# Optimization experiments

Hardware: AMD Instinct MI355X
Metric: run time of the kernel (lower is better)

Reference implementation:

```python
import jax, jax.numpy as jnp
import numpy as np

NOISE_MULTIPLIER = 1.1
L2_NORM_CLIP = 1.0


def setup_inputs() -> dict:
    key = jax.random.key(0)
    inputs = jax.random.normal(key, (16384, 1024), dtype=jnp.float32)
    return {"inputs": inputs}


def reference(inputs) -> jnp.ndarray:
    B = inputs.shape[0]
    embed_flat = inputs.reshape(B, -1)  # [B, D]
    # per-sample L2 norm; scale = 1 / max(norm / clip, 1)
    norm = jnp.linalg.norm(embed_flat, ord=2, axis=-1)  # [B]
    scale = 1.0 / jnp.maximum(norm / L2_NORM_CLIP, 1.0)  # [B]
    # row-wise scaling == diag(scale) @ embed_flat, without the O(B^2) matmul
    clipped = (embed_flat * scale[:, None]).reshape(inputs.shape)
    noise_key = jax.random.key(42)
    noise = NOISE_MULTIPLIER * L2_NORM_CLIP * jax.random.normal(
        noise_key, inputs.shape, dtype=inputs.dtype
    )
    return clipped + noise
```

## Files before the change

kernel.cpp:

```cpp
#include <hip/hip_runtime.h>
#include <cstdint>
#include <cstddef>

#define ROWS 16384
#define COLS 1024

__device__ __forceinline__ uint32_t rotl32(uint32_t x, int r) {
    return __builtin_amdgcn_alignbit(x, x, 32 - r);
}

struct TF4 { uint32_t a0,a1,b0,b1,c0,c1,d0,d1; };

__device__ __forceinline__ void tf_round4(TF4& s, int r) {
    s.a0 += s.a1; s.b0 += s.b1; s.c0 += s.c1; s.d0 += s.d1;
    s.a1 = rotl32(s.a1, r) ^ s.a0;
    s.b1 = rotl32(s.b1, r) ^ s.b0;
    s.c1 = rotl32(s.c1, r) ^ s.c0;
    s.d1 = rotl32(s.d1, r) ^ s.d0;
}

__device__ __forceinline__ void inj4(TF4& s, uint32_t k0, uint32_t k1) {
    s.a0 += k0; s.b0 += k0; s.c0 += k0; s.d0 += k0;
    s.a1 += k1; s.b1 += k1; s.c1 += k1; s.d1 += k1;
}

__device__ __forceinline__ void inj4_x1(TF4& s, uint32_t k1) {
    s.a1 += k1; s.b1 += k1; s.c1 += k1; s.d1 += k1;
}

__device__ __forceinline__ uint4 threefry_bits4(uint32_t i) {
    const uint32_t ks1 = 42u;
    const uint32_t ks2 = 0x1BD11BF0u;

    TF4 s;
    s.a1 = i + 42u;  s.a0 = s.a1;
    s.b1 = i + 43u;  s.b0 = s.b1;
    s.c1 = i + 44u;  s.c0 = s.c1;
    s.d1 = i + 45u;  s.d0 = s.d1;
    s.a1 = rotl32(s.a1, 13) ^ s.a0;
    s.b1 = rotl32(s.b1, 13) ^ s.b0;
    s.c1 = rotl32(s.c1, 13) ^ s.c0;
    s.d1 = rotl32(s.d1, 13) ^ s.d0;
    tf_round4(s, 15); tf_round4(s, 26); tf_round4(s, 6);
    inj4(s, ks1, ks2 + 1u);
    tf_round4(s, 17); tf_round4(s, 29); tf_round4(s, 16); tf_round4(s, 24);
    inj4(s, ks2, 2u);
    tf_round4(s, 13); tf_round4(s, 15); tf_round4(s, 26); tf_round4(s, 6);
    inj4_x1(s, ks1 + 3u);
    tf_round4(s, 17); tf_round4(s, 29); tf_round4(s, 16); tf_round4(s, 24);
    inj4(s, ks1, ks2 + 4u);
    tf_round4(s, 13); tf_round4(s, 15); tf_round4(s, 26); tf_round4(s, 6);
    inj4(s, ks2, 5u);

    return make_uint4(s.a0 ^ s.a1, s.b0 ^ s.b1, s.c0 ^ s.c1, s.d0 ^ s.d1);
}

__device__ __noinline__ float noise_tail(float y) {
    float w = fmaf(-0.69314718f, y, 2.5f);
    float s = __builtin_amdgcn_sqrtf(w) - 3.0f;
    float q = -3.1146030e-04f;
    q = fmaf(q, s, 1.5704224e-04f);
    q = fmaf(q, s, 2.0990855e-03f);
    q = fmaf(q, s, -5.7144932e-03f);
    q = fmaf(q, s, 8.9285939e-03f);
    q = fmaf(q, s, -1.1857797e-02f);
    q = fmaf(q, s, 1.4683435e-02f);
    q = fmaf(q, s, 1.5582439e+00f);
    q = fmaf(q, s, 4.4070777e+00f);
    return q;
}

__device__ __forceinline__ float4 noise4(uint32_t idx0) {
    uint4 b = threefry_bits4(idx0);

    float f0 = (float)(b.x >> 9);
    float f1 = (float)(b.y >> 9);
    float f2 = (float)(b.z >> 9);
    float f3 = (float)(b.w >> 9);

    const float S = 2.3841858e-07f;
    const float M = -0.99999994f;
    float v0 = fmaf(f0, S, M), v1 = fmaf(f1, S, M),
          v2 = fmaf(f2, S, M), v3 = fmaf(f3, S, M);

    float t0 = fmaf(-v0, v0, 1.0f), t1 = fmaf(-v1, v1, 1.0f),
          t2 = fmaf(-v2, v2, 1.0f), t3 = fmaf(-v3, v3, 1.0f);

    const float C = 3.6067376f;
    float y0 = __log2f(t0) + C, y1 = __log2f(t1) + C,
          y2 = __log2f(t2) + C, y3 = __log2f(t3) + C;

    const float K4 = 7.84913e-05f, K3 = 6.49511e-04f, K2 = -3.12243e-03f,
                K1 = -2.6594862e-01f, K0 = 2.3356449e+00f;
    float p0 = fmaf(K4, y0, K3), p1 = fmaf(K4, y1, K3),
          p2 = fmaf(K4, y2, K3), p3 = fmaf(K4, y3, K3);
    p0 = fmaf(p0, y0, K2); p1 = fmaf(p1, y1, K2);
    p2 = fmaf(p2, y2, K2); p3 = fmaf(p3, y3, K2);
    p0 = fmaf(p0, y0, K1); p1 = fmaf(p1, y1, K1);
    p2 = fmaf(p2, y2, K1); p3 = fmaf(p3, y3, K1);
    p0 = fmaf(p0, y0, K0); p1 = fmaf(p1, y1, K0);
    p2 = fmaf(p2, y2, K0); p3 = fmaf(p3, y3, K0);

    if (y0 <= -3.6067376f) p0 = noise_tail(y0);
    if (y1 <= -3.6067376f) p1 = noise_tail(y1);
    if (y2 <= -3.6067376f) p2 = noise_tail(y2);
    if (y3 <= -3.6067376f) p3 = noise_tail(y3);

    float4 n;
    n.x = p0 * v0; n.y = p1 * v1; n.z = p2 * v2; n.w = p3 * v3;
    return n;
}

__device__ __forceinline__ float ssq4(float4 a) {
    return fmaf(a.x, a.x, fmaf(a.y, a.y, fmaf(a.z, a.z, a.w * a.w)));
}

__global__ void __launch_bounds__(256)
gaussian_dp_kernel(const float* __restrict__ in, float* __restrict__ out) {
    const int wid  = threadIdx.x >> 6;
    const int lane = threadIdx.x & 63;
    const int r    = (blockIdx.x << 2) + wid;

    const float4* inR = reinterpret_cast<const float4*>(in + (size_t)r * COLS);
    float4 a0 = inR[lane];
    float4 a1 = inR[lane + 64];
    float4 a2 = inR[lane + 128];
    float4 a3 = inR[lane + 192];

    const uint32_t base = ((uint32_t)r << 10) + ((uint32_t)lane << 2);

    float4 n0 = noise4(base);
    float4 n1 = noise4(base + 256u);
    float4 n2 = noise4(base + 512u);
    float4 n3 = noise4(base + 768u);

    float ssq = (ssq4(a0) + ssq4(a1)) + (ssq4(a2) + ssq4(a3));

    #pragma unroll
    for (int off = 32; off > 0; off >>= 1) {
        ssq += __shfl_xor(ssq, off, 64);
    }

    const float scale = 1.0f / fmaxf(__builtin_amdgcn_sqrtf(ssq), 1.0f);

    float4* outR = reinterpret_cast<float4*>(out + (size_t)r * COLS);

    float4 o;
    o.x = fmaf(a0.x, scale, n0.x); o.y = fmaf(a0.y, scale, n0.y);
    o.z = fmaf(a0.z, scale, n0.z); o.w = fmaf(a0.w, scale, n0.w);
    outR[lane] = o;

    o.x = fmaf(a1.x, scale, n1.x); o.y = fmaf(a1.y, scale, n1.y);
    o.z = fmaf(a1.z, scale, n1.z); o.w = fmaf(a1.w, scale, n1.w);
    outR[lane + 64] = o;

    o.x = fmaf(a2.x, scale, n2.x); o.y = fmaf(a2.y, scale, n2.y);
    o.z = fmaf(a2.z, scale, n2.z); o.w = fmaf(a2.w, scale, n2.w);
    outR[lane + 128] = o;

    o.x = fmaf(a3.x, scale, n3.x); o.y = fmaf(a3.y, scale, n3.y);
    o.z = fmaf(a3.z, scale, n3.z); o.w = fmaf(a3.w, scale, n3.w);
    outR[lane + 192] = o;
}

extern "C" void kernel_launch(void* const* d_in, const int* in_sizes, int n_in,
                              void* d_out, int out_size, void* d_ws, size_t ws_size,
                              hipStream_t stream) {
    const float* in = (const float*)d_in[0];
    float* out = (float*)d_out;
    gaussian_dp_kernel<<<ROWS / 4, 256, 0, stream>>>(in, out);
}
```

Before: 40.50 us.

## Two-pass row processing with rolled loops and folded log offset in noise polynomial

The kernel now reads each row once to compute the sum of squares, then re-reads the input (expected to hit cache) and generates noise one float4 group at a time in a non-unrolled loop. This shrinks live state and register pressure, aiming for higher occupancy. It also folds the +C offset of the log2 value into the polynomial coefficients and the tail threshold, removing one add per element. The costs are a second read of the input and less instruction-level parallelism, since noise generation no longer overlaps the loads.

```diff
diff --git a/kernel.cpp b/kernel.cpp
--- a/kernel.cpp
+++ b/kernel.cpp
@@ -55,8 +55,8 @@
     return make_uint4(s.a0 ^ s.a1, s.b0 ^ s.b1, s.c0 ^ s.c1, s.d0 ^ s.d1);
 }
 
-__device__ __noinline__ float noise_tail(float y) {
-    float w = fmaf(-0.69314718f, y, 2.5f);
+__device__ __noinline__ float noise_tail(float L) {
+    float w = -0.69314718f * L;
     float s = __builtin_amdgcn_sqrtf(w) - 3.0f;
     float q = -3.1146030e-04f;
     q = fmaf(q, s, 1.5704224e-04f);
@@ -86,25 +86,24 @@
     float t0 = fmaf(-v0, v0, 1.0f), t1 = fmaf(-v1, v1, 1.0f),
           t2 = fmaf(-v2, v2, 1.0f), t3 = fmaf(-v3, v3, 1.0f);
 
-    const float C = 3.6067376f;
-    float y0 = __log2f(t0) + C, y1 = __log2f(t1) + C,
-          y2 = __log2f(t2) + C, y3 = __log2f(t3) + C;
+    float L0 = __log2f(t0), L1 = __log2f(t1),
+          L2 = __log2f(t2), L3 = __log2f(t3);
 
-    const float K4 = 7.84913e-05f, K3 = 6.49511e-04f, K2 = -3.12243e-03f,
-                K1 = -2.6594862e-01f, K0 = 2.3356449e+00f;
-    float p0 = fmaf(K4, y0, K3), p1 = fmaf(K4, y1, K3),
-          p2 = fmaf(K4, y2, K3), p3 = fmaf(K4, y3, K3);
-    p0 = fmaf(p0, y0, K2); p1 = fmaf(p1, y1, K2);
-    p2 = fmaf(p2, y2, K2); p3 = fmaf(p3, y3, K2);
-    p0 = fmaf(p0, y0, K1); p1 = fmaf(p1, y1, K1);
-    p2 = fmaf(p2, y2, K1); p3 = fmaf(p3, y3, K1);
-    p0 = fmaf(p0, y0, K0); p1 = fmaf(p1, y1, K0);
-    p2 = fmaf(p2, y2, K0); p3 = fmaf(p3, y3, K0);
+    const float K4 = 7.84913e-05f, K3 = 1.781908e-03f, K2 = 1.0031874e-02f,
+                K1 = -2.4839395e-01f, K0 = 1.3795727e+00f;
+    float p0 = fmaf(K4, L0, K3), p1 = fmaf(K4, L1, K3),
+          p2 = fmaf(K4, L2, K3), p3 = fmaf(K4, L3, K3);
+    p0 = fmaf(p0, L0, K2); p1 = fmaf(p1, L1, K2);
+    p2 = fmaf(p2, L2, K2); p3 = fmaf(p3, L3, K2);
+    p0 = fmaf(p0, L0, K1); p1 = fmaf(p1, L1, K1);
+    p2 = fmaf(p2, L2, K1); p3 = fmaf(p3, L3, K1);
+    p0 = fmaf(p0, L0, K0); p1 = fmaf(p1, L1, K0);
+    p2 = fmaf(p2, L2, K0); p3 = fmaf(p3, L3, K0);
 
-    if (y0 <= -3.6067376f) p0 = noise_tail(y0);
-    if (y1 <= -3.6067376f) p1 = noise_tail(y1);
-    if (y2 <= -3.6067376f) p2 = noise_tail(y2);
-    if (y3 <= -3.6067376f) p3 = noise_tail(y3);
+    if (L0 <= -7.2134752f) p0 = noise_tail(L0);
+    if (L1 <= -7.2134752f) p1 = noise_tail(L1);
+    if (L2 <= -7.2134752f) p2 = noise_tail(L2);
+    if (L3 <= -7.2134752f) p3 = noise_tail(L3);
 
     float4 n;
     n.x = p0 * v0; n.y = p1 * v1; n.z = p2 * v2; n.w = p3 * v3;
@@ -121,20 +120,15 @@
     const int lane = threadIdx.x & 63;
     const int r    = (blockIdx.x << 2) + wid;
 
-    const float4* inR = reinterpret_cast<const float4*>(in + (size_t)r * COLS);
-    float4 a0 = inR[lane];
-    float4 a1 = inR[lane + 64];
-    float4 a2 = inR[lane + 128];
-    float4 a3 = inR[lane + 192];
+    const float4* inR  = reinterpret_cast<const float4*>(in  + (size_t)r * COLS) + lane;
+    float4*       outR = reinterpret_cast<float4*>(out + (size_t)r * COLS) + lane;
 
-    const uint32_t base = ((uint32_t)r << 10) + ((uint32_t)lane << 2);
-
-    float4 n0 = noise4(base);
-    float4 n1 = noise4(base + 256u);
-    float4 n2 = noise4(base + 512u);
-    float4 n3 = noise4(base + 768u);
-
-    float ssq = (ssq4(a0) + ssq4(a1)) + (ssq4(a2) + ssq4(a3));
+    float ssq = 0.0f;
+    #pragma unroll 1
+    for (int g = 0; g < 4; ++g) {
+        float4 a = inR[g << 6];
+        ssq += ssq4(a);
+    }
 
     #pragma unroll
     for (int off = 32; off > 0; off >>= 1) {
@@ -143,24 +137,19 @@
 
     const float scale = 1.0f / fmaxf(__builtin_amdgcn_sqrtf(ssq), 1.0f);
 
-    float4* outR = reinterpret_cast<float4*>(out + (size_t)r * COLS);
+    const uint32_t base = ((uint32_t)r << 10) + ((uint32_t)lane << 2);
 
-    float4 o;
-    o.x = fmaf(a0.x, scale, n0.x); o.y = fmaf(a0.y, scale, n0.y);
-    o.z = fmaf(a0.z, scale, n0.z); o.w = fmaf(a0.w, scale, n0.w);
-    outR[lane] = o;
-
-    o.x = fmaf(a1.x, scale, n1.x); o.y = fmaf(a1.y, scale, n1.y);
-    o.z = fmaf(a1.z, scale, n1.z); o.w = fmaf(a1.w, scale, n1.w);
-    outR[lane + 64] = o;
-
-    o.x = fmaf(a2.x, scale, n2.x); o.y = fmaf(a2.y, scale, n2.y);
-    o.z = fmaf(a2.z, scale, n2.z); o.w = fmaf(a2.w, scale, n2.w);
-    outR[lane + 128] = o;
-
-    o.x = fmaf(a3.x, scale, n3.x); o.y = fmaf(a3.y, scale, n3.y);
-    o.z = fmaf(a3.z, scale, n3.z); o.w = fmaf(a3.w, scale, n3.w);
-    outR[lane + 192] = o;
+    #pragma unroll 1
+    for (int g = 0; g < 4; ++g) {
+        float4 a = inR[g << 6];
+        float4 n = noise4(base + ((uint32_t)g << 8));
+        float4 o;
+        o.x = fmaf(a.x, scale, n.x);
+        o.y = fmaf(a.y, scale, n.y);
+        o.z = fmaf(a.z, scale, n.z);
+        o.w = fmaf(a.w, scale, n.w);
+        outR[g << 6] = o;
+    }
 }
 
 extern "C" void kernel_launch(void* const* d_in, const int* in_sizes, int n_in,
```

Result: slower. 52.97 us (+30.8%).
